# Kernel optimization log

Measured on AMD Instinct MI355X. Metric: run time of the kernel, lower is better.

## Reference

```python
import jax, jax.numpy as jnp
import numpy as np

B, C, H, W = 4, 64, 96, 96
O = 64          # out_channel
K = 9           # 3x3 kernel positions
PAD = 1


def conv3x3(x, w, b):
    # NCHW 3x3 conv, stride 1, pad 1
    y = jax.lax.conv_general_dilated(
        x, w, window_strides=(1, 1), padding=((PAD, PAD), (PAD, PAD)),
        dimension_numbers=("NCHW", "OIHW", "NCHW"))
    return y + b[None, :, None, None]


def deform_conv3x3(x, offset, w, b):
    """torchvision-style DeformConv2d, 3x3, stride 1, pad 1, 1 offset group.
    x: [B, Cin, H, W]; offset: [B, 2*K, H, W] ordered (dy, dx) per kernel pos.
    """
    Bb, Cin, Hh, Ww = x.shape
    off = offset.reshape(Bb, K, 2, Hh, Ww)
    ky, kx = jnp.meshgrid(jnp.arange(3), jnp.arange(3), indexing="ij")
    ky = ky.reshape(K).astype(x.dtype)
    kx = kx.reshape(K).astype(x.dtype)
    hh = jnp.arange(Hh, dtype=x.dtype)
    ww = jnp.arange(Ww, dtype=x.dtype)
    # sampling coords: p0 + p_k + delta_p  -> [B, K, H, W]
    py = hh[None, None, :, None] - PAD + ky[None, :, None, None] + off[:, :, 0]
    px = ww[None, None, None, :] - PAD + kx[None, :, None, None] + off[:, :, 1]

    y0 = jnp.floor(py).astype(jnp.int32)
    x0 = jnp.floor(px).astype(jnp.int32)
    dy = py - y0.astype(x.dtype)
    dx = px - x0.astype(x.dtype)

    x_flat = x.reshape(Bb, Cin, Hh * Ww)

    def gather(yi, xi, wgt):
        valid = ((yi >= 0) & (yi < Hh) & (xi >= 0) & (xi < Ww)).astype(x.dtype)
        idx = (jnp.clip(yi, 0, Hh - 1) * Ww + jnp.clip(xi, 0, Ww - 1)).reshape(Bb, -1)
        vals = jax.vmap(lambda xf, ix: xf[:, ix])(x_flat, idx)  # [B, Cin, K*H*W]
        return vals * (wgt * valid).reshape(Bb, 1, -1)

    sampled = (gather(y0,     x0,     (1 - dy) * (1 - dx))
             + gather(y0,     x0 + 1, (1 - dy) * dx)
             + gather(y0 + 1, x0,     dy * (1 - dx))
             + gather(y0 + 1, x0 + 1, dy * dx))
    sampled = sampled.reshape(Bb, Cin, K, Hh, Ww)
    out = jnp.einsum("bckhw,ock->bohw", sampled, w.reshape(O, Cin, K))
    return out + b[None, :, None, None]


def setup_inputs() -> dict:
    key = jax.random.key(0)
    ks = jax.random.split(key, 6)
    ref_feat = jax.random.normal(ks[0], (B, C, H, W), dtype=jnp.float32)
    dist_feat = jax.random.normal(ks[1], (B, C, H, W), dtype=jnp.float32)
    offset_w = jax.random.normal(ks[2], (2 * K, C, 3, 3), dtype=jnp.float32) * 0.01
    offset_b = jnp.zeros((2 * K,), dtype=jnp.float32)
    deform_w = jax.random.normal(ks[3], (O, 3 * C, 3, 3), dtype=jnp.float32) * 0.05
    deform_b = jax.random.normal(ks[4], (O,), dtype=jnp.float32) * 0.05
    return {"ref_feat": ref_feat, "dist_feat": dist_feat,
            "offset_w": offset_w, "offset_b": offset_b,
            "deform_w": deform_w, "deform_b": deform_b}


def reference(ref_feat, dist_feat, offset_w, offset_b, deform_w, deform_b):
    offset = conv3x3(ref_feat, offset_w, offset_b)
    diff = (ref_feat - dist_feat) ** 2
    feat_in = jnp.concatenate((ref_feat, dist_feat, diff), axis=1)  # [B, 3C, H, W]
    feat = deform_conv3x3(feat_in, offset, deform_w, deform_b)
    feat = jax.nn.relu(feat)
    return (feat, diff)
```

## Files before the change

kernel.cpp:

```cpp
#include <hip/hip_runtime.h>
#include <hip/hip_fp16.h>

#define Wd    96
#define Hd    96
#define HW    9216
#define Bn    4
#define Cn    64
#define C3    192
#define On    64
#define NPIX  (Bn*HW)
#define NFEAT (Bn*Cn*HW)
#define NWTB  (9*6*4*512)
#define NWTB2 (18*2*64*8)
#define NRB3  (Bn*(HW/32))

#define HR2   6
#define HC    21
#define NPR2  (HR2*HC)
#define SELEM (NPR2*24)
#define HALO16 3072
#define HALO_B (HALO16*16)
#define NFBLK 1152

typedef __attribute__((ext_vector_type(8))) short s8v;
typedef __attribute__((ext_vector_type(8))) _Float16 h8v;
typedef __attribute__((ext_vector_type(4))) unsigned int u4v;
typedef __attribute__((ext_vector_type(4))) float f4v;

__device__ __forceinline__ unsigned packh(float lo, float hi) {
    __half2 h = __floats2half2_rn(lo, hi);
    return __builtin_bit_cast(unsigned, h);
}

__device__ __forceinline__ void gload_lds16(const void* g, void* l) {
    __builtin_amdgcn_global_load_lds(
        (const __attribute__((address_space(1))) unsigned int*)g,
        (__attribute__((address_space(3))) unsigned int*)l, 16, 0, 0);
}

__global__ __launch_bounds__(256) void repack_wts_kernel(
        const float* __restrict__ ref,
        const float* __restrict__ dist,
        unsigned int* __restrict__ packed,
        float* __restrict__ out_diff,
        const float* __restrict__ dw,
        const float* __restrict__ ow,
        __half* __restrict__ wtb,
        __half* __restrict__ wtb2) {
    __shared__ unsigned lds[96][33];

    int tid = threadIdx.x;

    if (blockIdx.x >= NRB3) {
        int e = (int)(blockIdx.x - NRB3) * 256 + tid;
        if (e < NWTB) {
            int j = e & 7;
            int L = (e >> 3) & 63;
            int mt = (e >> 9) & 3;
            int rest = e >> 11;
            int kc = rest % 6;
            int tap = rest / 6;
            int o = mt * 16 + (L & 15);
            int c = kc * 32 + (L >> 4) * 8 + j;
            wtb[e] = __float2half(dw[((size_t)o * C3 + c) * 9 + tap]);
        } else if (e < NWTB + NWTB2) {
            int e2 = e - NWTB;
            int j = e2 & 7;
            int L = (e2 >> 3) & 63;
            int mt = (e2 >> 9) & 1;
            int kc2 = e2 >> 10;
            int v = mt * 16 + (L & 15);
            int k = kc2 * 32 + ((L >> 4) & 3) * 8 + j;
            int c = k & 63;
            int tap = k >> 6;
            float val = (v < 18) ? ow[((size_t)v * Cn + c) * 9 + tap] : 0.f;
            wtb2[e2] = __float2half(val);
        }
        return;
    }

    int blk = blockIdx.x;
    int b = blk / (HW / 32);
    int pb = (blk - b * (HW / 32)) * 32;
    int pxg = tid & 7;
    int chp = tid >> 3;

    size_t base0 = ((size_t)(b * Cn + 2 * chp)) * HW + pb + pxg * 4;
    size_t base1 = base0 + HW;

    f4v r0 = *(const f4v*)(ref + base0);
    f4v r1 = *(const f4v*)(ref + base1);
    f4v d0 = *(const f4v*)(dist + base0);
    f4v d1 = *(const f4v*)(dist + base1);

    f4v q0 = (r0 - d0) * (r0 - d0);
    f4v q1 = (r1 - d1) * (r1 - d1);
    *(f4v*)(out_diff + base0) = q0;
    *(f4v*)(out_diff + base1) = q1;

#pragma unroll
    for (int j = 0; j < 4; ++j) {
        int p = pxg * 4 + j;
        lds[chp][p]      = packh(r0[j], r1[j]);
        lds[32 + chp][p] = packh(d0[j], d1[j]);
        lds[64 + chp][p] = packh(q0[j], q1[j]);
    }
    __syncthreads();

    {
        int p = tid >> 3;
        int part = tid & 7;
        unsigned* pko = packed + ((size_t)(b * HW + pb) + p) * 96 + part * 12;
#pragma unroll
        for (int q = 0; q < 3; ++q) {
            u4v w;
#pragma unroll
            for (int j = 0; j < 4; ++j)
                w[j] = lds[part * 12 + q * 4 + j][p];
            *(u4v*)(pko + q * 4) = w;
        }
    }
}

struct Ctx {
    int o00, o01, o10, o11;
    int l00, l01, l10, l11;
    float W00, W01, W10, W11;
    int inh;
};

__device__ __forceinline__ Ctx mkctx(int t, int y, int x, int xb, int yb,
                                     float2 o2) {
    Ctx c;
    float py = (float)(y - 1 + t / 3) + o2.x;
    float pxs = (float)(x - 1 + t % 3) + o2.y;
    float fy = floorf(py), fx = floorf(pxs);
    int y0 = (int)fy, x0 = (int)fx;
    int y1 = y0 + 1, x1 = x0 + 1;
    float ay = py - fy, ax = pxs - fx;
    bool vy0 = (unsigned)y0 < (unsigned)Hd;
    bool vy1 = (unsigned)y1 < (unsigned)Hd;
    bool vx0 = (unsigned)x0 < (unsigned)Wd;
    bool vx1 = (unsigned)x1 < (unsigned)Wd;
    c.W00 = (vy0 && vx0) ? (1.f - ay) * (1.f - ax) : 0.f;
    c.W01 = (vy0 && vx1) ? (1.f - ay) * ax : 0.f;
    c.W10 = (vy1 && vx0) ? ay * (1.f - ax) : 0.f;
    c.W11 = (vy1 && vx1) ? ay * ax : 0.f;
    int y0c = min(max(y0, 0), Hd - 1), y1c = min(max(y1, 0), Hd - 1);
    int x0c = min(max(x0, 0), Wd - 1), x1c = min(max(x1, 0), Wd - 1);
    c.o00 = (y0c * Wd + x0c) * (C3 * 2);
    c.o01 = (y0c * Wd + x1c) * (C3 * 2);
    c.o10 = (y1c * Wd + x0c) * (C3 * 2);
    c.o11 = (y1c * Wd + x1c) * (C3 * 2);
    int iy0 = y0c - yb + 2, iy1 = y1c - yb + 2;
    int ix0 = x0c - xb + 3, ix1 = x1c - xb + 3;
    c.inh = ((unsigned)iy0 < (unsigned)HR2) & ((unsigned)iy1 < (unsigned)HR2) &
            ((unsigned)ix0 < (unsigned)HC) & ((unsigned)ix1 < (unsigned)HC);
    int p00 = iy0 * HC + ix0, p01 = iy0 * HC + ix1;
    int p10 = iy1 * HC + ix0, p11 = iy1 * HC + ix1;
    c.l00 = p00 * 384 + (p00 & 7);
    c.l01 = p01 * 384 + (p01 & 7);
    c.l10 = p10 * 384 + (p10 & 7);
    c.l11 = p11 * 384 + (p11 & 7);
    return c;
}

__device__ __forceinline__ __half2 uh2(unsigned u) {
    return __builtin_bit_cast(__half2, u);
}

__device__ __forceinline__ void bilin_mfma(const s8v* rw, const Ctx& cc,
        const s8v* __restrict__ Ap, int t, int kb, int L, f4v* acc) {
    __half2 w00 = __float2half2_rn(cc.W00);
    __half2 w01 = __float2half2_rn(cc.W01);
    __half2 w10 = __float2half2_rn(cc.W10);
    __half2 w11 = __float2half2_rn(cc.W11);
#pragma unroll
    for (int i = 0; i < 3; ++i) {
        int kc = kb + i;
        u4v u00 = __builtin_bit_cast(u4v, rw[0 * 3 + i]);
        u4v u01 = __builtin_bit_cast(u4v, rw[1 * 3 + i]);
        u4v u10 = __builtin_bit_cast(u4v, rw[2 * 3 + i]);
        u4v u11 = __builtin_bit_cast(u4v, rw[3 * 3 + i]);
        u4v bu;
#pragma unroll
        for (int p = 0; p < 4; ++p) {
            __half2 v = __hmul2(uh2(u00[p]), w00);
            v = __hfma2(uh2(u01[p]), w01, v);
            v = __hfma2(uh2(u10[p]), w10, v);
            v = __hfma2(uh2(u11[p]), w11, v);
            bu[p] = __builtin_bit_cast(unsigned, v);
        }
        h8v bfrag = __builtin_bit_cast(h8v, bu);
#pragma unroll
        for (int mt = 0; mt < 4; ++mt) {
            h8v a = __builtin_bit_cast(h8v, Ap[((t * 6 + kc) * 4 + mt) * 64 + L]);
            acc[mt] = __builtin_amdgcn_mfma_f32_16x16x32_f16(a, bfrag, acc[mt], 0, 0, 0);
        }
    }
}

__global__ __launch_bounds__(384, 4) void fused_mfma(
        const __half* __restrict__ packed,
        const __half* __restrict__ wtb2,
        const float* __restrict__ ob,
        const __half* __restrict__ wtb,
        const float* __restrict__ db,
        float* __restrict__ out) {
    __shared__ __align__(16) char smem[HALO_B + 2 * 16 * 18 * 4];
    float (*off_l)[18] = (float(*)[18])(smem + HALO_B);
    float* redB = (float*)smem;

    int tid = threadIdx.x;
    int L = tid & 63;
    int wv = tid >> 6;
    int g  = wv / 3;
    int kv = wv - g * 3;
    int px = L & 15;
    int lg = L >> 4;
    int blk = blockIdx.x;
    int region = (blk & 7) * 144 + (blk >> 3);
    int b = region / 288;
    int rt = region - b * 288;
    int yt = rt / 6;
    int xt = rt - yt * 6;
    int yb = yt * 2, xb = xt * 16;
    int y = yb + g, x = xb + px;
    int pb = y * Wd + xb;
    int tbase = kv * 3;

    const char* pkb = (const char*)packed + (size_t)b * HW * (C3 * 2);
    const char* hb = (const char*)smem;

#pragma unroll
    for (int s = 0; s < 8; ++s) {
        int gi = tid + s * 384;
        int giS = min(gi, SELEM - 1);
        int pr = giS / 24;
        int slot = giS - pr * 24;
        int chblk = slot ^ (pr & 7);
        int iy = pr / HC, ix = pr - iy * HC;
        int gy = min(max(yb - 2 + iy, 0), Hd - 1);
        int gx = min(max(xb - 3 + ix, 0), Wd - 1);
        gload_lds16(pkb + ((size_t)(gy * Wd + gx)) * 384 + chblk * 16,
                    (char*)smem + (size_t)gi * 16);
    }
    __syncthreads();

    if (kv == 0) {
        const s8v* Ap = (const s8v*)wtb2;
        f4v acc0 = {0.f, 0.f, 0.f, 0.f};
        f4v acc1 = {0.f, 0.f, 0.f, 0.f};
#pragma unroll
        for (int t = 0; t < 9; ++t) {
            int ty = t / 3, tx = t - ty * 3;
            int yy = y - 1 + ty, xx = x - 1 + tx;
            bool val = (unsigned)yy < (unsigned)Hd && (unsigned)xx < (unsigned)Wd;
            short m = val ? (short)-1 : (short)0;
            int pr = (g + 1 + ty) * HC + (px + 2 + tx);
            int pbase = pr * 384;
            int key = pr & 7;
#pragma unroll
            for (int kc = 0; kc < 2; ++kc) {
                int chblk = kc * 4 + lg;
                s8v braw = *(const s8v*)(hb + pbase + ((chblk ^ key) << 4)) & m;
                h8v bfrag = __builtin_bit_cast(h8v, braw);
                h8v a0 = __builtin_bit_cast(h8v, Ap[((t * 2 + kc) * 2 + 0) * 64 + L]);
                h8v a1 = __builtin_bit_cast(h8v, Ap[((t * 2 + kc) * 2 + 1) * 64 + L]);
                acc0 = __builtin_amdgcn_mfma_f32_16x16x32_f16(a0, bfrag, acc0, 0, 0, 0);
                acc1 = __builtin_amdgcn_mfma_f32_16x16x32_f16(a1, bfrag, acc1, 0, 0, 0);
            }
        }
#pragma unroll
        for (int r = 0; r < 4; ++r) {
            int v = lg * 4 + r;
            off_l[g * 16 + px][v] = acc0[r] + ob[v];
        }
        if (lg == 0) {
#pragma unroll
            for (int r = 0; r < 2; ++r)
                off_l[g * 16 + px][16 + r] = acc1[r] + ob[16 + r];
        }
    }
    __syncthreads();

    const s8v* Ap = (const s8v*)wtb;

    Ctx ctx[3];
    int ok = 1;
#pragma unroll
    for (int tt = 0; tt < 3; ++tt) {
        int t = tbase + tt;
        float2 o2 = {off_l[g * 16 + px][2 * t], off_l[g * 16 + px][2 * t + 1]};
        ctx[tt] = mkctx(t, y, x, xb, yb, o2);
        ok &= ctx[tt].inh;
    }

    f4v acc[4];
    acc[0] = acc[1] = acc[2] = acc[3] = (f4v){0.f, 0.f, 0.f, 0.f};

    if (__all(ok)) {
#pragma unroll
        for (int h = 0; h < 6; ++h) {
            int tt = h >> 1;
            int t = tbase + tt;
            int kb = (h & 1) * 3;
            const Ctx cc = ctx[tt];
            int b00 = cc.l00 & ~127, k00 = cc.l00 & 7;
            int b01 = cc.l01 & ~127, k01 = cc.l01 & 7;
            int b10 = cc.l10 & ~127, k10 = cc.l10 & 7;
            int b11 = cc.l11 & ~127, k11 = cc.l11 & 7;
            s8v rw[12];
#pragma unroll
            for (int i = 0; i < 3; ++i) {
                int cb = (kb + i) * 4 + lg;
                rw[0 * 3 + i] = *(const s8v*)(hb + b00 + ((cb ^ k00) << 4));
                rw[1 * 3 + i] = *(const s8v*)(hb + b01 + ((cb ^ k01) << 4));
                rw[2 * 3 + i] = *(const s8v*)(hb + b10 + ((cb ^ k10) << 4));
                rw[3 * 3 + i] = *(const s8v*)(hb + b11 + ((cb ^ k11) << 4));
            }
            bilin_mfma(rw, cc, Ap, t, kb, L, acc);
        }
    } else {
#pragma unroll
        for (int h = 0; h < 6; ++h) {
            int tt = h >> 1;
            int t = tbase + tt;
            int kb = (h & 1) * 3;
            const Ctx cc = ctx[tt];
            s8v rw[12];
#pragma unroll
            for (int i = 0; i < 3; ++i) {
                int co = ((kb + i) * 4 + lg) * 16;
                rw[0 * 3 + i] = *(const s8v*)(pkb + cc.o00 + co);
                rw[1 * 3 + i] = *(const s8v*)(pkb + cc.o01 + co);
                rw[2 * 3 + i] = *(const s8v*)(pkb + cc.o10 + co);
                rw[3 * 3 + i] = *(const s8v*)(pkb + cc.o11 + co);
            }
            bilin_mfma(rw, cc, Ap, t, kb, L, acc);
        }
    }

    __syncthreads();
    if (kv != 0) {
        float* r = redB + ((g * 2 + kv - 1) * 64 + L) * 17;
#pragma unroll
        for (int mt = 0; mt < 4; ++mt)
#pragma unroll
            for (int q = 0; q < 4; ++q)
                r[mt * 4 + q] = acc[mt][q];
    }
    __syncthreads();
    if (kv == 0) {
        const float* r0 = redB + ((g * 2 + 0) * 64 + L) * 17;
        const float* r1 = redB + ((g * 2 + 1) * 64 + L) * 17;
#pragma unroll
        for (int mt = 0; mt < 4; ++mt) {
#pragma unroll
            for (int q = 0; q < 4; ++q) {
                int o = mt * 16 + lg * 4 + q;
                float v = acc[mt][q] + r0[mt * 4 + q] + r1[mt * 4 + q] + db[o];
                out[((size_t)(b * On + o)) * HW + pb + px] = fmaxf(v, 0.f);
            }
        }
    }
}

extern "C" void kernel_launch(void* const* d_in, const int* in_sizes, int n_in,
                              void* d_out, int out_size, void* d_ws, size_t ws_size,
                              hipStream_t stream) {
    const float* ref  = (const float*)d_in[0];
    const float* dist = (const float*)d_in[1];
    const float* ow   = (const float*)d_in[2];
    const float* ob   = (const float*)d_in[3];
    const float* dw   = (const float*)d_in[4];
    const float* db   = (const float*)d_in[5];

    float* out = (float*)d_out;

    __half* ws_wtb  = (__half*)d_ws;
    __half* ws_wtb2 = ws_wtb + NWTB;
    __half* ws_pk   = ws_wtb2 + NWTB2;

    int wts_blocks = (NWTB + NWTB2 + 255) / 256;
    repack_wts_kernel<<<NRB3 + wts_blocks, 256, 0, stream>>>(
        ref, dist, (unsigned int*)ws_pk, out + NFEAT, dw, ow, ws_wtb, ws_wtb2);
    fused_mfma<<<NFBLK, 384, 0, stream>>>(
        ws_pk, ws_wtb2, ob, ws_wtb, db, out);
}
```

Baseline: 116.8 us.

## Split LDS halo into channel sections and overlap offset conv with remaining loads

Reorganizes the LDS halo tile into three channel sections (128 bytes per pixel each) so the first section, needed by the offset conv, is loaded first. A partial vmcnt wait plus barrier then lets the offset MFMA start while the other sections are still arriving. The global-memory slow path now recomputes its addresses on the fly to cut register pressure, and s_setprio is raised around the main bilinear/MFMA loop. This relies on the global_load_lds ordering and the vmcnt accounting being exactly right, and there is no explicit wait for the remaining loads before the second phase reads them.

```diff
diff --git a/kernel.cpp b/kernel.cpp
--- a/kernel.cpp
+++ b/kernel.cpp
@@ -17,9 +17,11 @@
 #define HR2   6
 #define HC    21
 #define NPR2  (HR2*HC)
-#define SELEM (NPR2*24)
-#define HALO16 3072
-#define HALO_B (HALO16*16)
+#define SECT_SL 1008
+#define SECT_B  16128
+#define SELEM   3024
+#define HALO16  3072
+#define HALO_B  (HALO16*16)
 #define NFBLK 1152
 
 typedef __attribute__((ext_vector_type(8))) short s8v;
@@ -122,16 +124,15 @@
     }
 }
 
-struct Ctx {
-    int o00, o01, o10, o11;
+struct CtxF {
     int l00, l01, l10, l11;
     float W00, W01, W10, W11;
     int inh;
 };
 
-__device__ __forceinline__ Ctx mkctx(int t, int y, int x, int xb, int yb,
-                                     float2 o2) {
-    Ctx c;
+__device__ __forceinline__ CtxF mkctx_fast(int t, int y, int x, int xb, int yb,
+                                           float2 o2) {
+    CtxF c;
     float py = (float)(y - 1 + t / 3) + o2.x;
     float pxs = (float)(x - 1 + t % 3) + o2.y;
     float fy = floorf(py), fx = floorf(pxs);
@@ -148,20 +149,16 @@
     c.W11 = (vy1 && vx1) ? ay * ax : 0.f;
     int y0c = min(max(y0, 0), Hd - 1), y1c = min(max(y1, 0), Hd - 1);
     int x0c = min(max(x0, 0), Wd - 1), x1c = min(max(x1, 0), Wd - 1);
-    c.o00 = (y0c * Wd + x0c) * (C3 * 2);
-    c.o01 = (y0c * Wd + x1c) * (C3 * 2);
-    c.o10 = (y1c * Wd + x0c) * (C3 * 2);
-    c.o11 = (y1c * Wd + x1c) * (C3 * 2);
     int iy0 = y0c - yb + 2, iy1 = y1c - yb + 2;
     int ix0 = x0c - xb + 3, ix1 = x1c - xb + 3;
     c.inh = ((unsigned)iy0 < (unsigned)HR2) & ((unsigned)iy1 < (unsigned)HR2) &
             ((unsigned)ix0 < (unsigned)HC) & ((unsigned)ix1 < (unsigned)HC);
     int p00 = iy0 * HC + ix0, p01 = iy0 * HC + ix1;
     int p10 = iy1 * HC + ix0, p11 = iy1 * HC + ix1;
-    c.l00 = p00 * 384 + (p00 & 7);
-    c.l01 = p01 * 384 + (p01 & 7);
-    c.l10 = p10 * 384 + (p10 & 7);
-    c.l11 = p11 * 384 + (p11 & 7);
+    c.l00 = p00 * 128 + (p00 & 7);
+    c.l01 = p01 * 128 + (p01 & 7);
+    c.l10 = p10 * 128 + (p10 & 7);
+    c.l11 = p11 * 128 + (p11 & 7);
     return c;
 }
 
@@ -169,12 +166,13 @@
     return __builtin_bit_cast(__half2, u);
 }
 
-__device__ __forceinline__ void bilin_mfma(const s8v* rw, const Ctx& cc,
+__device__ __forceinline__ void bilin_mfma(const s8v* rw,
+        float W00, float W01, float W10, float W11,
         const s8v* __restrict__ Ap, int t, int kb, int L, f4v* acc) {
-    __half2 w00 = __float2half2_rn(cc.W00);
-    __half2 w01 = __float2half2_rn(cc.W01);
-    __half2 w10 = __float2half2_rn(cc.W10);
-    __half2 w11 = __float2half2_rn(cc.W11);
+    __half2 w00 = __float2half2_rn(W00);
+    __half2 w01 = __float2half2_rn(W01);
+    __half2 w10 = __float2half2_rn(W10);
+    __half2 w11 = __float2half2_rn(W11);
 #pragma unroll
     for (int i = 0; i < 3; ++i) {
         int kc = kb + i;
@@ -232,20 +230,35 @@
     const char* pkb = (const char*)packed + (size_t)b * HW * (C3 * 2);
     const char* hb = (const char*)smem;
 
-#pragma unroll
-    for (int s = 0; s < 8; ++s) {
-        int gi = tid + s * 384;
-        int giS = min(gi, SELEM - 1);
-        int pr = giS / 24;
-        int slot = giS - pr * 24;
-        int chblk = slot ^ (pr & 7);
-        int iy = pr / HC, ix = pr - iy * HC;
-        int gy = min(max(yb - 2 + iy, 0), Hd - 1);
-        int gx = min(max(xb - 3 + ix, 0), Wd - 1);
-        gload_lds16(pkb + ((size_t)(gy * Wd + gx)) * 384 + chblk * 16,
-                    (char*)smem + (size_t)gi * 16);
-    }
-    __syncthreads();
+    {
+        auto stage_one = [&](int Sdst, int Ssrc) {
+            int sec = (Ssrc >= 2 * SECT_SL) ? 2 : (Ssrc >= SECT_SL ? 1 : 0);
+            int rem = Ssrc - sec * SECT_SL;
+            int pr = rem >> 3, sl = rem & 7;
+            int chb = sec * 8 + (sl ^ (pr & 7));
+            int iy = pr / HC, ix = pr - iy * HC;
+            int gy = min(max(yb - 2 + iy, 0), Hd - 1);
+            int gx = min(max(xb - 3 + ix, 0), Wd - 1);
+            gload_lds16(pkb + ((size_t)(gy * Wd + gx)) * 384 + chb * 16,
+                        (char*)smem + (size_t)Sdst * 16);
+        };
+        __builtin_amdgcn_sched_barrier(0);
+#pragma unroll
+        for (int r = 0; r < 3; ++r) {
+            int S = tid + r * 384;
+            stage_one(S, S);
+        }
+        __builtin_amdgcn_sched_barrier(0);
+#pragma unroll
+        for (int r = 0; r < 5; ++r) {
+            int S = 1152 + tid + r * 384;
+            stage_one(S, min(S, SELEM - 1));
+        }
+    }
+    __builtin_amdgcn_sched_barrier(0);
+    asm volatile("s_waitcnt vmcnt(5)" ::: "memory");
+    __builtin_amdgcn_s_barrier();
+    __builtin_amdgcn_sched_barrier(0);
 
     if (kv == 0) {
         const s8v* Ap = (const s8v*)wtb2;
@@ -258,12 +271,12 @@
             bool val = (unsigned)yy < (unsigned)Hd && (unsigned)xx < (unsigned)Wd;
             short m = val ? (short)-1 : (short)0;
             int pr = (g + 1 + ty) * HC + (px + 2 + tx);
-            int pbase = pr * 384;
+            int pbase = pr * 128;
             int key = pr & 7;
 #pragma unroll
             for (int kc = 0; kc < 2; ++kc) {
-                int chblk = kc * 4 + lg;
-                s8v braw = *(const s8v*)(hb + pbase + ((chblk ^ key) << 4)) & m;
+                int chb = kc * 4 + lg;
+                s8v braw = *(const s8v*)(hb + pbase + ((chb ^ key) << 4)) & m;
                 h8v bfrag = __builtin_bit_cast(h8v, braw);
                 h8v a0 = __builtin_bit_cast(h8v, Ap[((t * 2 + kc) * 2 + 0) * 64 + L]);
                 h8v a1 = __builtin_bit_cast(h8v, Ap[((t * 2 + kc) * 2 + 1) * 64 + L]);
@@ -286,26 +299,29 @@
 
     const s8v* Ap = (const s8v*)wtb;
 
-    Ctx ctx[3];
+    float2 o2a[3];
+    CtxF ctx[3];
     int ok = 1;
 #pragma unroll
     for (int tt = 0; tt < 3; ++tt) {
         int t = tbase + tt;
-        float2 o2 = {off_l[g * 16 + px][2 * t], off_l[g * 16 + px][2 * t + 1]};
-        ctx[tt] = mkctx(t, y, x, xb, yb, o2);
+        o2a[tt].x = off_l[g * 16 + px][2 * t];
+        o2a[tt].y = off_l[g * 16 + px][2 * t + 1];
+        ctx[tt] = mkctx_fast(t, y, x, xb, yb, o2a[tt]);
         ok &= ctx[tt].inh;
     }
 
     f4v acc[4];
     acc[0] = acc[1] = acc[2] = acc[3] = (f4v){0.f, 0.f, 0.f, 0.f};
 
+    __builtin_amdgcn_s_setprio(1);
     if (__all(ok)) {
 #pragma unroll
         for (int h = 0; h < 6; ++h) {
             int tt = h >> 1;
             int t = tbase + tt;
             int kb = (h & 1) * 3;
-            const Ctx cc = ctx[tt];
+            const CtxF cc = ctx[tt];
             int b00 = cc.l00 & ~127, k00 = cc.l00 & 7;
             int b01 = cc.l01 & ~127, k01 = cc.l01 & 7;
             int b10 = cc.l10 & ~127, k10 = cc.l10 & 7;
@@ -313,33 +329,45 @@
             s8v rw[12];
 #pragma unroll
             for (int i = 0; i < 3; ++i) {
-                int cb = (kb + i) * 4 + lg;
-                rw[0 * 3 + i] = *(const s8v*)(hb + b00 + ((cb ^ k00) << 4));
-                rw[1 * 3 + i] = *(const s8v*)(hb + b01 + ((cb ^ k01) << 4));
-                rw[2 * 3 + i] = *(const s8v*)(hb + b10 + ((cb ^ k10) << 4));
-                rw[3 * 3 + i] = *(const s8v*)(hb + b11 + ((cb ^ k11) << 4));
+                int secoff = ((kb + i) >> 1) * SECT_B;
+                int chb3 = ((kb + i) & 1) * 4 + lg;
+                rw[0 * 3 + i] = *(const s8v*)(hb + secoff + b00 + ((chb3 ^ k00) << 4));
+                rw[1 * 3 + i] = *(const s8v*)(hb + secoff + b01 + ((chb3 ^ k01) << 4));
+                rw[2 * 3 + i] = *(const s8v*)(hb + secoff + b10 + ((chb3 ^ k10) << 4));
+                rw[3 * 3 + i] = *(const s8v*)(hb + secoff + b11 + ((chb3 ^ k11) << 4));
             }
-            bilin_mfma(rw, cc, Ap, t, kb, L, acc);
+            bilin_mfma(rw, cc.W00, cc.W01, cc.W10, cc.W11, Ap, t, kb, L, acc);
         }
     } else {
 #pragma unroll
-        for (int h = 0; h < 6; ++h) {
-            int tt = h >> 1;
+        for (int tt = 0; tt < 3; ++tt) {
             int t = tbase + tt;
-            int kb = (h & 1) * 3;
-            const Ctx cc = ctx[tt];
-            s8v rw[12];
-#pragma unroll
-            for (int i = 0; i < 3; ++i) {
-                int co = ((kb + i) * 4 + lg) * 16;
-                rw[0 * 3 + i] = *(const s8v*)(pkb + cc.o00 + co);
-                rw[1 * 3 + i] = *(const s8v*)(pkb + cc.o01 + co);
-                rw[2 * 3 + i] = *(const s8v*)(pkb + cc.o10 + co);
-                rw[3 * 3 + i] = *(const s8v*)(pkb + cc.o11 + co);
+            float py = (float)(y - 1 + t / 3) + o2a[tt].x;
+            float pxs = (float)(x - 1 + t % 3) + o2a[tt].y;
+            float fy = floorf(py), fx = floorf(pxs);
+            int y0 = (int)fy, x0 = (int)fx;
+            int y0c = min(max(y0, 0), Hd - 1), y1c = min(max(y0 + 1, 0), Hd - 1);
+            int x0c = min(max(x0, 0), Wd - 1), x1c = min(max(x0 + 1, 0), Wd - 1);
+            int o00 = (y0c * Wd + x0c) * 384, o01 = (y0c * Wd + x1c) * 384;
+            int o10 = (y1c * Wd + x0c) * 384, o11 = (y1c * Wd + x1c) * 384;
+#pragma unroll
+            for (int half = 0; half < 2; ++half) {
+                int kb = half * 3;
+                s8v rw[12];
+#pragma unroll
+                for (int i = 0; i < 3; ++i) {
+                    int co = ((kb + i) * 4 + lg) * 16;
+                    rw[0 * 3 + i] = *(const s8v*)(pkb + o00 + co);
+                    rw[1 * 3 + i] = *(const s8v*)(pkb + o01 + co);
+                    rw[2 * 3 + i] = *(const s8v*)(pkb + o10 + co);
+                    rw[3 * 3 + i] = *(const s8v*)(pkb + o11 + co);
+                }
+                bilin_mfma(rw, ctx[tt].W00, ctx[tt].W01, ctx[tt].W10, ctx[tt].W11,
+                           Ap, t, kb, L, acc);
             }
-            bilin_mfma(rw, cc, Ap, t, kb, L, acc);
-        }
-    }
+        }
+    }
+    __builtin_amdgcn_s_setprio(0);
 
     __syncthreads();
     if (kv != 0) {
```

Result: no change. 116.3 us, median of 3 (-0.4%).
